# Performance work log

Measured on AMD Instinct MI355X. Metric: run time of the kernel, lower is better.

The kernel has to match this reference:

```python
import jax, jax.numpy as jnp
import numpy as np
import math

NUM_GROUPS = 32
EPS = 1e-5


def setup_inputs() -> dict:
    key = jax.random.key(0)
    k1, k2, k3 = jax.random.split(key, 3)
    B, C, H, W = 8, 128, 64, 64
    x = jax.random.normal(k1, (B, C, H, W), dtype=jnp.float32)
    gn_w = jnp.ones((C,), dtype=jnp.float32)
    gn_b = jnp.zeros((C,), dtype=jnp.float32)
    # 1x1 conv -> dense weight [3C, C] (kernel dims squeezed)
    qkv_w = jax.random.normal(k2, (3 * C, C), dtype=jnp.float32) * (1.0 / math.sqrt(C))
    qkv_b = jax.random.normal(k3, (3 * C,), dtype=jnp.float32) * 0.01
    return {"x": x, "gn_w": gn_w, "gn_b": gn_b, "qkv_w": qkv_w, "qkv_b": qkv_b}


def _group_norm(x, w, b):
    B, C, H, W = x.shape
    xg = x.reshape(B, NUM_GROUPS, C // NUM_GROUPS, H, W)
    mean = xg.mean(axis=(2, 3, 4), keepdims=True)
    var = xg.var(axis=(2, 3, 4), keepdims=True)
    xn = ((xg - mean) * jax.lax.rsqrt(var + EPS)).reshape(B, C, H, W)
    return xn * w[None, :, None, None] + b[None, :, None, None]


def reference(x, gn_w, gn_b, qkv_w, qkv_b):
    B, C, H, W = x.shape
    scale = 1.0 / math.sqrt(C)
    h = _group_norm(x, gn_w, gn_b)
    # 1x1 conv == channel-mixing matmul: [B, 3C, H*W]
    hf = h.reshape(B, C, H * W)
    qkv = jnp.einsum('oc,bcs->bos', qkv_w, hf) + qkv_b[None, :, None]
    q, k, v = jnp.split(qkv, 3, axis=1)  # each [B, C, S]
    attn = jnp.einsum('bct,bcs->bts', q, k) * scale  # [B, S, S]
    attn = jax.nn.softmax(attn, axis=2)
    a = jnp.einsum('bts,bcs->bct', attn, v)  # [B, C, S]
    return x * a.reshape(B, C, H, W)
```

## Files before the change

kernel.cpp:

```cpp
#include <hip/hip_runtime.h>
#include <hip/hip_bf16.h>
#include <stdint.h>

typedef unsigned short u16;
typedef unsigned int   u32;
typedef __attribute__((ext_vector_type(8)))  short bf16x8;
typedef __attribute__((ext_vector_type(8)))  unsigned short u16x8;
typedef __attribute__((ext_vector_type(4)))  float f32x4;
typedef __attribute__((ext_vector_type(16))) float f32x16;

#define SC2 0.1275174475f

#define MFMA3216(A, B, C) __builtin_amdgcn_mfma_f32_32x32x16_bf16(A, B, C, 0, 0, 0)
#define MFMA1632(A, B, C) __builtin_amdgcn_mfma_f32_16x16x32_bf16(A, B, C, 0, 0, 0)

__device__ __forceinline__ float bf2f(u16 u) {
    union { u32 i; float f; } t; t.i = ((u32)u) << 16; return t.f;
}
__device__ __forceinline__ u16 f2bf(float f) {
    union { u32 i; float f; } t; t.f = f;
    u32 b = t.i;
    return (u16)((b + 0x7fffu + ((b >> 16) & 1u)) >> 16);
}
__device__ __forceinline__ u32 packbf(float a, float b) {
    union { __hip_bfloat162 h; u32 u; } c;
    c.h = __float22bfloat162_rn(float2{a, b});
    return c.u;
}

__device__ __forceinline__ void gload16(const u16* g, u16* l) {
    __builtin_amdgcn_global_load_lds(
        (const __attribute__((address_space(1))) void*)g,
        (__attribute__((address_space(3))) void*)l, 16, 0, 0);
}

__global__ __launch_bounds__(256) void stats_kernel(
    const float* __restrict__ x, const float* __restrict__ gw,
    const float* __restrict__ gb, float* __restrict__ gp, float* __restrict__ bp)
{
    int b = blockIdx.x & 7, g = blockIdx.x >> 3;
    long base = ((long)(b * 128 + g * 4)) << 12;
    const float4* x4 = (const float4*)(x + base);

    float s = 0.f, ss = 0.f;
    for (int i = threadIdx.x; i < 4096; i += 256) {
        float4 v = x4[i];
        s  += v.x + v.y + v.z + v.w;
        ss += v.x * v.x + v.y * v.y + v.z * v.z + v.w * v.w;
    }
    #pragma unroll
    for (int off = 32; off > 0; off >>= 1) {
        s  += __shfl_xor(s,  off);
        ss += __shfl_xor(ss, off);
    }
    __shared__ float red[8];
    int wid = threadIdx.x >> 6;
    if ((threadIdx.x & 63) == 0) { red[wid * 2] = s; red[wid * 2 + 1] = ss; }
    __syncthreads();
    s  = red[0] + red[2] + red[4] + red[6];
    ss = red[1] + red[3] + red[5] + red[7];

    float mean = s * (1.f / 16384.f);
    float var  = ss * (1.f / 16384.f) - mean * mean;
    float rs   = rsqrtf(var + 1e-5f);

    if (threadIdx.x < 4) {
        int c = g * 4 + threadIdx.x;
        float gamma = gw[c] * rs;
        gp[b * 128 + c] = gamma;
        bp[b * 128 + c] = gb[c] - mean * gamma;
    }
}

__global__ __launch_bounds__(256) void wconv_kernel(
    const float* __restrict__ w, u16* __restrict__ wbf)
{
    int idx = (blockIdx.x * 256 + threadIdx.x) * 4;
    float4 v = *(const float4*)&w[idx];
    ushort4 o = { f2bf(v.x), f2bf(v.y), f2bf(v.z), f2bf(v.w) };
    *(ushort4*)&wbf[idx] = o;
}

__global__ __launch_bounds__(256) void qkvm_kernel(
    const float* __restrict__ x, const float* __restrict__ gp,
    const float* __restrict__ bp, const u16* __restrict__ wbf,
    const float* __restrict__ bias,
    u16* __restrict__ Qt, u16* __restrict__ Kt, u16* __restrict__ Vv)
{
    __shared__ u16 ldsH[64 * 128];
    __shared__ float gpl[128], bpl[128];
    int tid = threadIdx.x, lane = tid & 63, wv = tid >> 6;
    int g = lane >> 4, t = lane & 15;
    int b = blockIdx.x & 7, stile = blockIdx.x >> 3;
    int s0 = stile << 6;

    if (tid < 128) { gpl[tid] = gp[b * 128 + tid]; bpl[tid] = bp[b * 128 + tid]; }
    __syncthreads();

    const float* xb = x + ((long)b << 19);
    int sl = tid & 63, cq = tid >> 6;
    #pragma unroll
    for (int c8 = 0; c8 < 4; ++c8) {
        int CH = cq * 4 + c8;
        u16 tmp[8];
        #pragma unroll
        for (int j = 0; j < 8; ++j) {
            int c = CH * 8 + j;
            float v = xb[((long)c << 12) + s0 + sl];
            tmp[j] = f2bf(v * gpl[c] + bpl[c]);
        }
        *(u16x8*)&ldsH[sl * 128 + ((CH ^ (sl & 15)) << 3)] = *(u16x8*)tmp;
    }
    __syncthreads();

    bf16x8 hf[4];
    int slq = (wv << 4) + t;
    #pragma unroll
    for (int ks = 0; ks < 4; ++ks)
        hf[ks] = *(const bf16x8*)&ldsH[slq * 128 + ((((ks << 2) + g) ^ t) << 3)];

    u16* Qtb = Qt + ((long)b << 19);
    u16* Ktb = Kt + ((long)b << 19);
    u16* Vb  = Vv + ((long)b << 19);
    int srow = s0 + (wv << 4) + (g << 2);

    #pragma unroll
    for (int ot = 0; ot < 8; ++ot) {
        bf16x8 wf[4];
        #pragma unroll
        for (int ks = 0; ks < 4; ++ks)
            wf[ks] = *(const bf16x8*)&wbf[(ot * 16 + t) * 128 + ks * 32 + g * 8];
        float bv = bias[ot * 16 + t];
        f32x4 acc = (f32x4){bv, bv, bv, bv};
        #pragma unroll
        for (int ks = 0; ks < 4; ++ks)
            acc = MFMA1632(hf[ks], wf[ks], acc);
        #pragma unroll
        for (int r = 0; r < 4; ++r)
            Qtb[(long)(srow + r) * 128 + ot * 16 + t] = f2bf(acc[r] * SC2);
    }
    #pragma unroll
    for (int ot = 8; ot < 16; ++ot) {
        bf16x8 wf[4];
        #pragma unroll
        for (int ks = 0; ks < 4; ++ks)
            wf[ks] = *(const bf16x8*)&wbf[(ot * 16 + t) * 128 + ks * 32 + g * 8];
        float bv = bias[ot * 16 + t];
        f32x4 acc = (f32x4){bv, bv, bv, bv};
        #pragma unroll
        for (int ks = 0; ks < 4; ++ks)
            acc = MFMA1632(hf[ks], wf[ks], acc);
        #pragma unroll
        for (int r = 0; r < 4; ++r)
            Ktb[(long)(srow + r) * 128 + (ot - 8) * 16 + t] = f2bf(acc[r]);
    }
    #pragma unroll
    for (int ot = 16; ot < 24; ++ot) {
        bf16x8 wf[4];
        #pragma unroll
        for (int ks = 0; ks < 4; ++ks)
            wf[ks] = *(const bf16x8*)&wbf[(ot * 16 + t) * 128 + ks * 32 + g * 8];
        float4 b4 = *(const float4*)&bias[ot * 16 + (g << 2)];
        f32x4 acc = (f32x4){b4.x, b4.y, b4.z, b4.w};
        #pragma unroll
        for (int ks = 0; ks < 4; ++ks)
            acc = MFMA1632(wf[ks], hf[ks], acc);
        #pragma unroll
        for (int r = 0; r < 4; ++r) {
            int cv = (ot - 16) * 16 + (g << 2) + r;
            Vb[((long)cv << 12) + s0 + (wv << 4) + t] = f2bf(acc[r]);
        }
    }
}

__global__ __launch_bounds__(256) void attn_kernel(
    const u16* __restrict__ Qt, const u16* __restrict__ Kt,
    const u16* __restrict__ Vv, const float* __restrict__ x,
    float* __restrict__ out)
{
    __shared__ u16 ldsAll[32768];
    u16* ldsK = ldsAll;
    u16* ldsV = ldsAll + 16384;

    int tid = threadIdx.x, lane = tid & 63, wv = tid >> 6;
    int wq = wv >> 1, wk = wv & 1;
    int q5 = lane & 31, h = lane >> 5;
    int b = blockIdx.x & 7, qb = blockIdx.x >> 3;
    int s0 = qb << 6;

    const u16* Qb = Qt + ((long)b << 19);
    const u16* Kb = Kt + ((long)b << 19);
    const u16* Vb = Vv + ((long)b << 19);

    bf16x8 qf[8];
    {
        long qrow = (long)(s0 + (wq << 5) + q5) << 7;
        #pragma unroll
        for (int d = 0; d < 8; ++d)
            qf[d] = *(const bf16x8*)&Qb[qrow + (d << 4) + (h << 3)];
    }

    f32x16 acco[4];
    #pragma unroll
    for (int cb = 0; cb < 4; ++cb)
        #pragma unroll
        for (int r = 0; r < 16; ++r) acco[cb][r] = 0.f;
    float llp = 0.f;

    u32 kso[4], vso[4];
    #pragma unroll
    for (int i = 0; i < 4; ++i) {
        int n = (((wv << 2) + i) << 6) + lane;
        {
            int s = n >> 4, ch = n & 15;
            kso[i] = s * 128 + ((ch ^ (s & 15)) << 3);
        }
        {
            int cpair = n >> 4, q = n & 15;
            int dec = q ^ (cpair & 15);
            int c = cpair * 2 + (dec >> 3);
            int ch8 = dec & 7;
            vso[i] = c * 4096 + (ch8 << 3);
        }
    }

    int sKey = (wk << 5) + q5;
    u32 kfo[8];
    #pragma unroll
    for (int d = 0; d < 8; ++d) {
        int ch = (d << 1) + h;
        kfo[d] = sKey * 128 + ((ch ^ (sKey & 15)) << 3);
    }
    u32 vfo[8];
    #pragma unroll
    for (int cb = 0; cb < 4; ++cb)
        #pragma unroll
        for (int ks = 0; ks < 2; ++ks) {
            int c = (cb << 5) + q5;
            int ch8 = (wk << 2) + (ks << 1) + h;
            int cpair = c >> 1;
            int q = (ch8 + ((c & 1) << 3)) ^ (cpair & 15);
            vfo[cb * 2 + ks] = cpair * 128 + (q << 3);
        }

    auto STAGE = [&](int buf) {
        #pragma unroll
        for (int i = 0; i < 4; ++i) {
            int seg = (wv << 2) + i;
            gload16(Kb + kso[i], &ldsK[(buf << 13) + (seg << 9)]);
            gload16(Vb + vso[i], &ldsV[(buf << 13) + (seg << 9)]);
            kso[i] += 8192;
            vso[i] += 64;
        }
    };

    auto ITER = [&](int buf, bool prefetch) {
        if (prefetch) STAGE(buf ^ 1);

        const u16* lK = ldsK + (buf << 13);
        const u16* lV = ldsV + (buf << 13);

        bf16x8 kf[8];
        #pragma unroll
        for (int d = 0; d < 8; ++d)
            kf[d] = *(const bf16x8*)&lK[kfo[d]];

        f32x16 s;
        #pragma unroll
        for (int r = 0; r < 16; ++r) s[r] = 0.f;
        __builtin_amdgcn_s_setprio(1);
        #pragma unroll
        for (int d = 0; d < 8; ++d)
            s = MFMA3216(kf[d], qf[d], s);
        __builtin_amdgcn_s_setprio(0);

        float e[16];
        #pragma unroll
        for (int r = 0; r < 16; ++r)
            e[r] = exp2f(s[r]);
        float s0a = (e[0] + e[1]) + (e[2] + e[3]);
        float s1a = (e[4] + e[5]) + (e[6] + e[7]);
        float s2a = (e[8] + e[9]) + (e[10] + e[11]);
        float s3a = (e[12] + e[13]) + (e[14] + e[15]);
        llp += (s0a + s1a) + (s2a + s3a);

        u32 pk0[2], pk1[2], pk2[2], pk3[2];
        pk0[0] = packbf(e[0],  e[1]);  pk0[1] = packbf(e[2],  e[3]);
        pk1[0] = packbf(e[4],  e[5]);  pk1[1] = packbf(e[6],  e[7]);
        pk2[0] = packbf(e[8],  e[9]);  pk2[1] = packbf(e[10], e[11]);
        pk3[0] = packbf(e[12], e[13]); pk3[1] = packbf(e[14], e[15]);
        u32 t0[2], t1[2];
        #pragma unroll
        for (int j = 0; j < 2; ++j) {
            t0[j] = (u32)__shfl_xor((int)(h ? pk0[j] : pk1[j]), 32);
            t1[j] = (u32)__shfl_xor((int)(h ? pk2[j] : pk3[j]), 32);
        }
        union { u32 u[4]; bf16x8 v; } pb0, pb1;
        pb0.u[0] = h ? t0[0]  : pk0[0];
        pb0.u[1] = h ? t0[1]  : pk0[1];
        pb0.u[2] = h ? pk1[0] : t0[0];
        pb0.u[3] = h ? pk1[1] : t0[1];
        pb1.u[0] = h ? t1[0]  : pk2[0];
        pb1.u[1] = h ? t1[1]  : pk2[1];
        pb1.u[2] = h ? pk3[0] : t1[0];
        pb1.u[3] = h ? pk3[1] : t1[1];

        __builtin_amdgcn_s_setprio(1);
        #pragma unroll
        for (int cb = 0; cb < 4; ++cb) {
            bf16x8 v0 = *(const bf16x8*)&lV[vfo[cb * 2 + 0]];
            acco[cb] = MFMA3216(v0, pb0.v, acco[cb]);
            bf16x8 v1 = *(const bf16x8*)&lV[vfo[cb * 2 + 1]];
            acco[cb] = MFMA3216(v1, pb1.v, acco[cb]);
        }
        __builtin_amdgcn_s_setprio(0);

        __syncthreads();
    };

    STAGE(0);
    __syncthreads();

    #pragma unroll 1
    for (int kt2 = 0; kt2 < 32; ++kt2) {
        ITER(0, true);
        ITER(1, kt2 < 31);
    }

    float ll = llp + __shfl_xor(llp, 32);
    float* mlsp = (float*)ldsAll;
    if (h == 0)
        mlsp[(((wq << 1) + wk) << 5) + q5] = ll;
    __syncthreads();
    float lo = mlsp[(((wq << 1) + (wk ^ 1)) << 5) + q5];
    float sc = 1.0f / (ll + lo);
    __syncthreads();

    float* mrg = (wk == 0) ? (float*)ldsAll : (float*)(ldsAll + 16384);
    #pragma unroll
    for (int cb = 0; cb < 4; ++cb)
        #pragma unroll
        for (int r = 0; r < 16; ++r) {
            int c = (cb << 5) + (r & 3) + ((r >> 2) << 3) + (h << 2);
            mrg[(c << 6) + (wq << 5) + q5] = acco[cb][r] * sc;
        }
    __syncthreads();

    const float* mA = (const float*)ldsAll;
    const float* mB = (const float*)(ldsAll + 16384);
    const float* xb = x + ((long)b << 19);
    float* ob = out + ((long)b << 19);
    int q6 = tid & 63, c0 = tid >> 6;
    #pragma unroll 8
    for (int i = 0; i < 32; ++i) {
        int c = (i << 2) + c0;
        float v = mA[(c << 6) + q6] + mB[(c << 6) + q6];
        long gi = ((long)c << 12) + s0 + q6;
        ob[gi] = xb[gi] * v;
    }
}

extern "C" void kernel_launch(void* const* d_in, const int* in_sizes, int n_in,
                              void* d_out, int out_size, void* d_ws, size_t ws_size,
                              hipStream_t stream)
{
    const float* x    = (const float*)d_in[0];
    const float* gw   = (const float*)d_in[1];
    const float* gb   = (const float*)d_in[2];
    const float* w    = (const float*)d_in[3];
    const float* bias = (const float*)d_in[4];
    float* out = (float*)d_out;

    u16* Qt  = (u16*)d_ws;
    u16* Kt  = Qt + (size_t)8 * 4096 * 128;
    u16* Vv  = Kt + (size_t)8 * 4096 * 128;
    u16* wbf = Vv + (size_t)8 * 128 * 4096;
    float* gp = (float*)(wbf + (size_t)384 * 128);
    float* bp = gp + 1024;

    stats_kernel<<<256, 256, 0, stream>>>(x, gw, gb, gp, bp);
    wconv_kernel<<<48, 256, 0, stream>>>(w, wbf);
    qkvm_kernel<<<512, 256, 0, stream>>>(x, gp, bp, wbf, bias, Qt, Kt, Vv);
    attn_kernel<<<512, 256, 0, stream>>>(Qt, Kt, Vv, x, out);
}
```

Measured before the change: 145.2 us.

## Restructure attention to 32-query blocks with direct global V reads, fuse prep kernels

The attention kernel now gives each block 32 queries split across 4 key-parallel waves instead of 64 queries over 2x2 waves. It drops the LDS double buffer for V, reading V fragments straight from global memory, and stages only K through LDS in a single buffer with syncs around each tile. The normalisation merge now sums four partial accumulators through LDS in two passes. The stats and weight-conversion kernels are fused into one launch to save launch overhead. The grid doubles to 1024 blocks and LDS use drops, at the cost of losing prefetch overlap, reading K twice as often overall, and issuing uncoalesced global V loads.

After: 237.0 us. 1.63x slower.

```diff
diff --git a/kernel.cpp b/kernel.cpp
--- a/kernel.cpp
+++ b/kernel.cpp
@@ -34,10 +34,18 @@
         (__attribute__((address_space(3))) void*)l, 16, 0, 0);
 }
 
-__global__ __launch_bounds__(256) void stats_kernel(
+__global__ __launch_bounds__(256) void prep_kernel(
     const float* __restrict__ x, const float* __restrict__ gw,
-    const float* __restrict__ gb, float* __restrict__ gp, float* __restrict__ bp)
+    const float* __restrict__ gb, float* __restrict__ gp, float* __restrict__ bp,
+    const float* __restrict__ w, u16* __restrict__ wbf)
 {
+    if (blockIdx.x >= 256) {
+        int idx = ((blockIdx.x - 256) * 256 + threadIdx.x) * 4;
+        float4 v = *(const float4*)&w[idx];
+        ushort4 o = { f2bf(v.x), f2bf(v.y), f2bf(v.z), f2bf(v.w) };
+        *(ushort4*)&wbf[idx] = o;
+        return;
+    }
     int b = blockIdx.x & 7, g = blockIdx.x >> 3;
     long base = ((long)(b * 128 + g * 4)) << 12;
     const float4* x4 = (const float4*)(x + base);
@@ -70,15 +78,6 @@
         gp[b * 128 + c] = gamma;
         bp[b * 128 + c] = gb[c] - mean * gamma;
     }
-}
-
-__global__ __launch_bounds__(256) void wconv_kernel(
-    const float* __restrict__ w, u16* __restrict__ wbf)
-{
-    int idx = (blockIdx.x * 256 + threadIdx.x) * 4;
-    float4 v = *(const float4*)&w[idx];
-    ushort4 o = { f2bf(v.x), f2bf(v.y), f2bf(v.z), f2bf(v.w) };
-    *(ushort4*)&wbf[idx] = o;
 }
 
 __global__ __launch_bounds__(256) void qkvm_kernel(
@@ -178,15 +177,13 @@
     const u16* __restrict__ Vv, const float* __restrict__ x,
     float* __restrict__ out)
 {
-    __shared__ u16 ldsAll[32768];
-    u16* ldsK = ldsAll;
-    u16* ldsV = ldsAll + 16384;
-
-    int tid = threadIdx.x, lane = tid & 63, wv = tid >> 6;
-    int wq = wv >> 1, wk = wv & 1;
+    __shared__ u16 ldsK[16384];
+    __shared__ float mls[4][32];
+
+    int tid = threadIdx.x, lane = tid & 63, wk = tid >> 6;
     int q5 = lane & 31, h = lane >> 5;
     int b = blockIdx.x & 7, qb = blockIdx.x >> 3;
-    int s0 = qb << 6;
+    int s0 = qb << 5;
 
     const u16* Qb = Qt + ((long)b << 19);
     const u16* Kb = Kt + ((long)b << 19);
@@ -194,7 +191,7 @@
 
     bf16x8 qf[8];
     {
-        long qrow = (long)(s0 + (wq << 5) + q5) << 7;
+        long qrow = (long)(s0 + q5) << 7;
         #pragma unroll
         for (int d = 0; d < 8; ++d)
             qf[d] = *(const bf16x8*)&Qb[qrow + (d << 4) + (h << 3)];
@@ -207,21 +204,12 @@
         for (int r = 0; r < 16; ++r) acco[cb][r] = 0.f;
     float llp = 0.f;
 
-    u32 kso[4], vso[4];
-    #pragma unroll
-    for (int i = 0; i < 4; ++i) {
-        int n = (((wv << 2) + i) << 6) + lane;
-        {
-            int s = n >> 4, ch = n & 15;
-            kso[i] = s * 128 + ((ch ^ (s & 15)) << 3);
-        }
-        {
-            int cpair = n >> 4, q = n & 15;
-            int dec = q ^ (cpair & 15);
-            int c = cpair * 2 + (dec >> 3);
-            int ch8 = dec & 7;
-            vso[i] = c * 4096 + (ch8 << 3);
-        }
+    u32 kso[8];
+    #pragma unroll
+    for (int i = 0; i < 8; ++i) {
+        int n = (((wk << 3) + i) << 6) + lane;
+        int key = n >> 4, ch = n & 15;
+        kso[i] = key * 128 + ((ch ^ (key & 15)) << 3);
     }
 
     int sKey = (wk << 5) + q5;
@@ -231,39 +219,27 @@
         int ch = (d << 1) + h;
         kfo[d] = sKey * 128 + ((ch ^ (sKey & 15)) << 3);
     }
-    u32 vfo[8];
+
+    u32 vgo[8];
     #pragma unroll
     for (int cb = 0; cb < 4; ++cb)
         #pragma unroll
-        for (int ks = 0; ks < 2; ++ks) {
-            int c = (cb << 5) + q5;
-            int ch8 = (wk << 2) + (ks << 1) + h;
-            int cpair = c >> 1;
-            int q = (ch8 + ((c & 1) << 3)) ^ (cpair & 15);
-            vfo[cb * 2 + ks] = cpair * 128 + (q << 3);
-        }
-
-    auto STAGE = [&](int buf) {
-        #pragma unroll
-        for (int i = 0; i < 4; ++i) {
-            int seg = (wv << 2) + i;
-            gload16(Kb + kso[i], &ldsK[(buf << 13) + (seg << 9)]);
-            gload16(Vb + vso[i], &ldsV[(buf << 13) + (seg << 9)]);
-            kso[i] += 8192;
-            vso[i] += 64;
-        }
-    };
-
-    auto ITER = [&](int buf, bool prefetch) {
-        if (prefetch) STAGE(buf ^ 1);
-
-        const u16* lK = ldsK + (buf << 13);
-        const u16* lV = ldsV + (buf << 13);
+        for (int ks = 0; ks < 2; ++ks)
+            vgo[cb * 2 + ks] = (u32)(((cb << 5) + q5) * 4096
+                                     + (wk << 5) + (ks << 4) + (h << 3));
+
+    for (int kt = 0; kt < 32; ++kt) {
+        #pragma unroll
+        for (int i = 0; i < 8; ++i) {
+            gload16(Kb + kso[i], &ldsK[(((wk << 3) + i)) << 9]);
+            kso[i] += 16384;
+        }
+        __syncthreads();
 
         bf16x8 kf[8];
         #pragma unroll
         for (int d = 0; d < 8; ++d)
-            kf[d] = *(const bf16x8*)&lK[kfo[d]];
+            kf[d] = *(const bf16x8*)&ldsK[kfo[d]];
 
         f32x16 s;
         #pragma unroll
@@ -308,55 +284,49 @@
         __builtin_amdgcn_s_setprio(1);
         #pragma unroll
         for (int cb = 0; cb < 4; ++cb) {
-            bf16x8 v0 = *(const bf16x8*)&lV[vfo[cb * 2 + 0]];
+            bf16x8 v0 = *(const bf16x8*)&Vb[vgo[cb * 2 + 0]];
             acco[cb] = MFMA3216(v0, pb0.v, acco[cb]);
-            bf16x8 v1 = *(const bf16x8*)&lV[vfo[cb * 2 + 1]];
+            bf16x8 v1 = *(const bf16x8*)&Vb[vgo[cb * 2 + 1]];
             acco[cb] = MFMA3216(v1, pb1.v, acco[cb]);
         }
         __builtin_amdgcn_s_setprio(0);
+        #pragma unroll
+        for (int j = 0; j < 8; ++j) vgo[j] += 128;
 
         __syncthreads();
-    };
-
-    STAGE(0);
+    }
+
+    float ll = llp + __shfl_xor(llp, 32);
+    if (h == 0) mls[wk][q5] = ll;
     __syncthreads();
-
-    #pragma unroll 1
-    for (int kt2 = 0; kt2 < 32; ++kt2) {
-        ITER(0, true);
-        ITER(1, kt2 < 31);
-    }
-
-    float ll = llp + __shfl_xor(llp, 32);
-    float* mlsp = (float*)ldsAll;
-    if (h == 0)
-        mlsp[(((wq << 1) + wk) << 5) + q5] = ll;
-    __syncthreads();
-    float lo = mlsp[(((wq << 1) + (wk ^ 1)) << 5) + q5];
-    float sc = 1.0f / (ll + lo);
-    __syncthreads();
-
-    float* mrg = (wk == 0) ? (float*)ldsAll : (float*)(ldsAll + 16384);
-    #pragma unroll
-    for (int cb = 0; cb < 4; ++cb)
-        #pragma unroll
-        for (int r = 0; r < 16; ++r) {
-            int c = (cb << 5) + (r & 3) + ((r >> 2) << 3) + (h << 2);
-            mrg[(c << 6) + (wq << 5) + q5] = acco[cb][r] * sc;
-        }
-    __syncthreads();
-
-    const float* mA = (const float*)ldsAll;
-    const float* mB = (const float*)(ldsAll + 16384);
+    float sc = 1.0f / ((mls[0][q5] + mls[1][q5]) + (mls[2][q5] + mls[3][q5]));
+
+    float* mrg = (float*)ldsK;
     const float* xb = x + ((long)b << 19);
     float* ob = out + ((long)b << 19);
-    int q6 = tid & 63, c0 = tid >> 6;
-    #pragma unroll 8
-    for (int i = 0; i < 32; ++i) {
-        int c = (i << 2) + c0;
-        float v = mA[(c << 6) + q6] + mB[(c << 6) + q6];
-        long gi = ((long)c << 12) + s0 + q6;
-        ob[gi] = xb[gi] * v;
+
+    #pragma unroll
+    for (int p = 0; p < 2; ++p) {
+        #pragma unroll
+        for (int cb2 = 0; cb2 < 2; ++cb2) {
+            int cb = (p << 1) + cb2;
+            #pragma unroll
+            for (int r = 0; r < 16; ++r) {
+                int cl = (cb2 << 5) + (r & 3) + ((r >> 2) << 3) + (h << 2);
+                mrg[(wk << 11) + (cl << 5) + q5] = acco[cb][r] * sc;
+            }
+        }
+        __syncthreads();
+        #pragma unroll
+        for (int j = 0; j < 8; ++j) {
+            int idx = (j << 8) + tid;
+            int cl = idx >> 5, q = idx & 31;
+            int o = (cl << 5) + q;
+            float sum = (mrg[o] + mrg[o + 2048]) + (mrg[o + 4096] + mrg[o + 6144]);
+            long gi = (((long)((p << 6) + cl)) << 12) + s0 + q;
+            ob[gi] = xb[gi] * sum;
+        }
+        if (p == 0) __syncthreads();
     }
 }
 
@@ -378,8 +348,7 @@
     float* gp = (float*)(wbf + (size_t)384 * 128);
     float* bp = gp + 1024;
 
-    stats_kernel<<<256, 256, 0, stream>>>(x, gw, gb, gp, bp);
-    wconv_kernel<<<48, 256, 0, stream>>>(w, wbf);
+    prep_kernel<<<304, 256, 0, stream>>>(x, gw, gb, gp, bp, w, wbf);
     qkvm_kernel<<<512, 256, 0, stream>>>(x, gp, bp, wbf, bias, Qt, Kt, Vv);
-    attn_kernel<<<512, 256, 0, stream>>>(Qt, Kt, Vv, x, out);
-}
+    attn_kernel<<<1024, 256, 0, stream>>>(Qt, Kt, Vv, x, out);
+}
```
